# Kernel optimization log

Hardware: AMD Instinct MI355X
Metric: run time of the kernel (lower is better)

The kernel has to match this reference:

```python
import jax, jax.numpy as jnp
import numpy as np

VOCAB = 50257
HIDDEN = 2048
B, S = 4, 8192
MAX_ROWS, MAX_COLS = 64, 64


def setup_inputs() -> dict:
    key = jax.random.key(0)
    k1, k2, k3, k4, k5, k6, k7 = jax.random.split(key, 7)
    input_ids = jax.random.randint(k1, (B, S), 0, VOCAB, dtype=jnp.int32)
    row_idx = jax.random.randint(k2, (B, S), 0, MAX_ROWS, dtype=jnp.int32)
    col_idx = jax.random.randint(k3, (B, S), 0, MAX_COLS, dtype=jnp.int32)
    grid_mask = jax.random.randint(k4, (B, S), 0, 2, dtype=jnp.int32).astype(jnp.bool_)
    emb_table = jax.random.normal(k5, (VOCAB, HIDDEN), dtype=jnp.float32) * 0.02
    row_vec = jax.random.normal(k6, (1, HIDDEN), dtype=jnp.float32) * 0.02
    col_vec = jax.random.normal(k7, (1, HIDDEN), dtype=jnp.float32) * 0.02
    return {"input_ids": input_ids, "row_idx": row_idx, "col_idx": col_idx,
            "grid_mask": grid_mask, "emb_table": emb_table,
            "row_vec": row_vec, "col_vec": col_vec}


def reference(input_ids, row_idx, col_idx, grid_mask, emb_table, row_vec, col_vec):
    # Token embedding lookup: [B, S, H]
    tok = emb_table[input_ids]
    # Scaled grid position embedding: pos(r, c) = (r+1)*row_vec + (c+1)*col_vec
    # (scaled_position_embedding=True path: row/col embeddings are single rows)
    r = (row_idx + 1).astype(tok.dtype)[..., None]  # [B, S, 1]
    c = (col_idx + 1).astype(tok.dtype)[..., None]  # [B, S, 1]
    pos = r * row_vec[0] + c * col_vec[0]            # [B, S, H]
    # Scatter semantics: only tokens inside a grid receive a position embed
    grid_embeds = jnp.where(grid_mask[..., None], pos, jnp.zeros((), tok.dtype))
    # Dropout with hidden_dropout_prob=0.0 (eval) is identity
    return tok + grid_embeds
```

## Files before the change

### kernel.cpp

```cpp
#include <hip/hip_runtime.h>
#include <hip/hip_bf16.h>


#define HIDDEN 2048
#define NTOK (4 * 8192)

__global__ __launch_bounds__(256) void GridEmbedding_64046552318105_kernel(
    const int* __restrict__ ids,
    const int* __restrict__ rows,
    const int* __restrict__ cols,
    const int* __restrict__ mask,
    const float* __restrict__ emb,
    const float* __restrict__ rvec,
    const float* __restrict__ cvec,
    float* __restrict__ out) {
    const int tok = blockIdx.x;
    const int t = threadIdx.x;

    const long long id = (long long)ids[tok];
    const float r = (float)(rows[tok] + 1);
    const float c = (float)(cols[tok] + 1);
    const bool m = mask[tok] != 0;

    const float4* __restrict__ src = reinterpret_cast<const float4*>(emb + id * HIDDEN);
    const float4* __restrict__ rv  = reinterpret_cast<const float4*>(rvec);
    const float4* __restrict__ cv  = reinterpret_cast<const float4*>(cvec);
    float4* __restrict__ dst = reinterpret_cast<float4*>(out + (long long)tok * HIDDEN);

    #pragma unroll
    for (int i = 0; i < 2; ++i) {
        const int j = t + i * 256;
        float4 e = src[j];
        if (m) {
            const float4 a = rv[j];
            const float4 b = cv[j];
            e.x += r * a.x + c * b.x;
            e.y += r * a.y + c * b.y;
            e.z += r * a.z + c * b.z;
            e.w += r * a.w + c * b.w;
        }
        dst[j] = e;
    }
}

extern "C" void kernel_launch(void* const* d_in, const int* in_sizes, int n_in,
                              void* d_out, int out_size, void* d_ws, size_t ws_size,
                              hipStream_t stream) {
    const int*   ids  = (const int*)d_in[0];
    const int*   rows = (const int*)d_in[1];
    const int*   cols = (const int*)d_in[2];
    const int*   mask = (const int*)d_in[3];
    const float* emb  = (const float*)d_in[4];
    const float* rvec = (const float*)d_in[5];
    const float* cvec = (const float*)d_in[6];
    float* out = (float*)d_out;

    GridEmbedding_64046552318105_kernel<<<NTOK, 256, 0, stream>>>(
        ids, rows, cols, mask, emb, rvec, cvec, out);
}
```

Baseline: 97.04 us.

## Map one wavefront per token with batched loads and nontemporal stores

Each 64-lane wavefront now handles a whole token row, so a block covers four tokens and the grid shrinks by four. All eight 16-byte loads per lane are issued before any compute, raising memory-level parallelism, and the output goes out through nontemporal stores so the write stream does not pollute cache. Per-token scalar index loads become wave-uniform. Register use rises with eight vector values held per lane.

```diff
diff --git a/kernel.cpp b/kernel.cpp
--- a/kernel.cpp
+++ b/kernel.cpp
@@ -4,6 +4,8 @@
 
 #define HIDDEN 2048
 #define NTOK (4 * 8192)
+
+typedef float vfloat4 __attribute__((ext_vector_type(4)));
 
 __global__ __launch_bounds__(256) void GridEmbedding_64046552318105_kernel(
     const int* __restrict__ ids,
@@ -14,33 +16,37 @@
     const float* __restrict__ rvec,
     const float* __restrict__ cvec,
     float* __restrict__ out) {
-    const int tok = blockIdx.x;
-    const int t = threadIdx.x;
+    const int wave = threadIdx.x >> 6;
+    const int lane = threadIdx.x & 63;
+    const int tok  = (blockIdx.x << 2) + wave;
 
     const long long id = (long long)ids[tok];
     const float r = (float)(rows[tok] + 1);
     const float c = (float)(cols[tok] + 1);
     const bool m = mask[tok] != 0;
 
-    const float4* __restrict__ src = reinterpret_cast<const float4*>(emb + id * HIDDEN);
-    const float4* __restrict__ rv  = reinterpret_cast<const float4*>(rvec);
-    const float4* __restrict__ cv  = reinterpret_cast<const float4*>(cvec);
-    float4* __restrict__ dst = reinterpret_cast<float4*>(out + (long long)tok * HIDDEN);
+    const vfloat4* __restrict__ src = reinterpret_cast<const vfloat4*>(emb + id * HIDDEN);
+    const vfloat4* __restrict__ rv  = reinterpret_cast<const vfloat4*>(rvec);
+    const vfloat4* __restrict__ cv  = reinterpret_cast<const vfloat4*>(cvec);
+    vfloat4* __restrict__ dst = reinterpret_cast<vfloat4*>(out + (long long)tok * HIDDEN);
+
+    vfloat4 e[8];
+    #pragma unroll
+    for (int i = 0; i < 8; ++i) e[i] = src[lane + i * 64];
+
+    if (m) {
+        #pragma unroll
+        for (int i = 0; i < 8; ++i) {
+            const int j = lane + i * 64;
+            const vfloat4 a = rv[j];
+            const vfloat4 b = cv[j];
+            e[i] += r * a + c * b;
+        }
+    }
 
     #pragma unroll
-    for (int i = 0; i < 2; ++i) {
-        const int j = t + i * 256;
-        float4 e = src[j];
-        if (m) {
-            const float4 a = rv[j];
-            const float4 b = cv[j];
-            e.x += r * a.x + c * b.x;
-            e.y += r * a.y + c * b.y;
-            e.z += r * a.z + c * b.z;
-            e.w += r * a.w + c * b.w;
-        }
-        dst[j] = e;
-    }
+    for (int i = 0; i < 8; ++i)
+        __builtin_nontemporal_store(e[i], &dst[lane + i * 64]);
 }
 
 extern "C" void kernel_launch(void* const* d_in, const int* in_sizes, int n_in,
@@ -55,6 +61,6 @@
     const float* cvec = (const float*)d_in[6];
     float* out = (float*)d_out;
 
-    GridEmbedding_64046552318105_kernel<<<NTOK, 256, 0, stream>>>(
+    GridEmbedding_64046552318105_kernel<<<NTOK / 4, 256, 0, stream>>>(
         ids, rows, cols, mask, emb, rvec, cvec, out);
 }
```

Result: faster. 82.50 us (-15.0%).
